# Kernel optimization log

Hardware: AMD Instinct MI355X
Metric: run time of the kernel (lower is better)

Reference implementation:

```python
import jax, jax.numpy as jnp
import numpy as np

NHID = 128
NLAYERS = 4
DT = 1.0
ALPHA = 1.0
GAMMA = 1.0


def setup_inputs() -> dict:
    key = jax.random.key(0)
    k1, k2, k3, k4, k5, k6 = jax.random.split(key, 6)
    N, E = 100000, 1600000
    stdv = 1.0 / np.sqrt(NHID)
    x = jax.random.normal(k1, (N, NHID), dtype=jnp.float32)
    edge_index = jax.random.randint(k2, (2, E), 0, N, dtype=jnp.int64)
    # GCNConv.lin weight (no bias) and separate conv bias; reset_params uniform(-stdv, stdv) for weights
    W = jax.random.uniform(k3, (NHID, NHID), jnp.float32, -stdv, stdv)
    b = jnp.zeros((NHID,), jnp.float32)
    Wres = jax.random.uniform(k4, (NHID, NHID), jnp.float32, -stdv, stdv)
    bres = jax.random.uniform(k5, (NHID,), jnp.float32, -stdv, stdv)
    return {"x": x, "edge_index": edge_index, "W": W, "b": b, "Wres": Wres, "bres": bres}


def reference(x, edge_index, W, b, Wres, bres):
    N = x.shape[0]
    src, dst = edge_index[0], edge_index[1]
    # GCN degree normalization with self-loops (A_hat = A + I)
    deg = jax.ops.segment_sum(jnp.ones(src.shape[0], x.dtype), dst, num_segments=N) + 1.0
    dinv = jax.lax.rsqrt(deg)  # deg >= 1 from self-loops

    def conv(X):
        h = X @ W  # lin (no bias)
        norm = (dinv[src] * dinv[dst])[:, None]
        msg = h[src] * norm                      # [E, nhid] gather
        agg = jax.ops.segment_sum(msg, dst, num_segments=N)  # scatter-add
        agg = agg + h * (dinv * dinv)[:, None]   # self-loop contribution
        return agg + b

    def residual(X):
        # res_connection_v1: -res(conv.lin(X))
        return -((X @ W) @ Wres + bres)

    # dropout is identity in eval mode
    Y = jnp.tanh(x)
    X = Y
    for _ in range(NLAYERS):
        Y = Y + DT * (jnp.tanh(conv(X) + residual(X)) - ALPHA * Y - GAMMA * X)
        X = X + DT * Y
    return X
```

## Files before the change

### kernel.cpp

```cpp
#include <hip/hip_runtime.h>
#include <hip/hip_bf16.h>
#include <stdint.h>

#define THREADS 256
#define WB 256
#define MAXNB 512
#define NBLK_A 512

typedef unsigned short u16;
typedef unsigned int u32;
using frag_ab = __attribute__((ext_vector_type(8))) short;
using f32x4  = __attribute__((ext_vector_type(4))) float;

static __host__ __device__ inline int imin(int a, int b) { return a < b ? a : b; }

static __device__ inline u16 f2b(float f) {
    u32 u = __builtin_bit_cast(u32, f);
    return (u16)((u + 0x7FFFu + ((u >> 16) & 1u)) >> 16);
}
static __device__ inline float b2f_lo(u32 v) { return __builtin_bit_cast(float, v << 16); }
static __device__ inline float b2f_hi(u32 v) { return __builtin_bit_cast(float, v & 0xFFFF0000u); }

static __device__ inline float tanh_fast(float x) {
    const float e = __builtin_amdgcn_exp2f(x * 2.8853900817779268f);
    return 1.0f - 2.0f * __builtin_amdgcn_rcpf(e + 1.0f);
}

static __device__ inline void fma8(float* a, float w, uint4 v) {
    a[0] = fmaf(w, b2f_lo(v.x), a[0]); a[1] = fmaf(w, b2f_hi(v.x), a[1]);
    a[2] = fmaf(w, b2f_lo(v.y), a[2]); a[3] = fmaf(w, b2f_hi(v.y), a[3]);
    a[4] = fmaf(w, b2f_lo(v.z), a[4]); a[5] = fmaf(w, b2f_hi(v.z), a[5]);
    a[6] = fmaf(w, b2f_lo(v.w), a[6]); a[7] = fmaf(w, b2f_hi(v.w), a[7]);
}

__global__ void k_detect(const int* __restrict__ raw, int* __restrict__ flag) {
    __shared__ int found;
    if (threadIdx.x == 0) found = 0;
    __syncthreads();
    if (raw[2 * threadIdx.x + 1] != 0) atomicOr(&found, 1);
    __syncthreads();
    if (threadIdx.x == 0) *flag = found ? 0 : 1;
}

__global__ __launch_bounds__(256)
void k_bucket_count(const int* __restrict__ raw, int E, int EPB, int NB,
                    const int* __restrict__ flag, int* __restrict__ counts) {
    __shared__ int cnt[MAXNB];
    const int t = threadIdx.x, blk = blockIdx.x;
    for (int i = t; i < NB; i += THREADS) cnt[i] = 0;
    __syncthreads();
    const bool is64 = (*flag != 0);
    const int e0 = blk * EPB, e1 = imin(E, e0 + EPB);
    for (int e = e0 + t; e < e1; e += THREADS) {
        const int d = is64 ? raw[2 * E + 2 * e] : raw[E + e];
        atomicAdd(&cnt[d >> 8], 1);
    }
    __syncthreads();
    for (int i = t; i < NB; i += THREADS) counts[i * NBLK_A + blk] = cnt[i];
}

__global__ void k_chunk_sums(const int* __restrict__ a, int* __restrict__ chunkSum, int L) {
    __shared__ int sm[THREADS];
    const int base = blockIdx.x * 2048 + threadIdx.x * 8;
    int s = 0;
#pragma unroll
    for (int i = 0; i < 8; ++i) { int idx = base + i; if (idx < L) s += a[idx]; }
    sm[threadIdx.x] = s;
    __syncthreads();
    for (int off = THREADS / 2; off > 0; off >>= 1) {
        if (threadIdx.x < off) sm[threadIdx.x] += sm[threadIdx.x + off];
        __syncthreads();
    }
    if (threadIdx.x == 0) chunkSum[blockIdx.x] = sm[0];
}

__global__ void k_scan_offsets(const int* __restrict__ chunkSum, int* __restrict__ chunkOff,
                               int nChunks) {
    if (blockIdx.x == 0 && threadIdx.x == 0) {
        int run = 0;
        for (int i = 0; i < nChunks; ++i) { chunkOff[i] = run; run += chunkSum[i]; }
    }
}

__global__ void k_scan_write(int* __restrict__ a, const int* __restrict__ chunkOff, int L) {
    __shared__ int sm[THREADS];
    const int tid = threadIdx.x;
    const int base = blockIdx.x * 2048 + tid * 8;
    int v[8]; int s = 0;
#pragma unroll
    for (int i = 0; i < 8; ++i) { int idx = base + i; v[i] = (idx < L) ? a[idx] : 0; s += v[i]; }
    const int mysum = s;
    sm[tid] = s;
    __syncthreads();
    for (int off = 1; off < THREADS; off <<= 1) {
        int t = (tid >= off) ? sm[tid - off] : 0;
        __syncthreads();
        sm[tid] += t;
        __syncthreads();
    }
    int run = chunkOff[blockIdx.x] + sm[tid] - mysum;
#pragma unroll
    for (int i = 0; i < 8; ++i) {
        int idx = base + i;
        if (idx < L) { a[idx] = run; run += v[i]; }
    }
}

__global__ __launch_bounds__(256)
void k_bucket_scatter(const int* __restrict__ raw, int E, int EPB, int NB,
                      const int* __restrict__ flag, const int* __restrict__ offs,
                      uint2* __restrict__ pairs) {
    __shared__ int cur[MAXNB];
    const int t = threadIdx.x, blk = blockIdx.x;
    for (int i = t; i < NB; i += THREADS) cur[i] = offs[i * NBLK_A + blk];
    __syncthreads();
    const bool is64 = (*flag != 0);
    const int e0 = blk * EPB, e1 = imin(E, e0 + EPB);
    for (int e = e0 + t; e < e1; e += THREADS) {
        int s, d;
        if (is64) { s = raw[2 * e]; d = raw[2 * E + 2 * e]; }
        else      { s = raw[e];     d = raw[E + e]; }
        const int p = atomicAdd(&cur[d >> 8], 1);
        pairs[p] = make_uint2((u32)s, (u32)d);
    }
}

__global__ __launch_bounds__(256)
void k_build(const uint2* __restrict__ pairs, const int* __restrict__ offs,
             int* __restrict__ rowptr, int* __restrict__ csr_src,
             float* __restrict__ dinv, int N, int NB, int E) {
    __shared__ int deg[WB];
    __shared__ int ptr[WB];
    __shared__ int cur[WB];
    const int k = blockIdx.x, t = threadIdx.x;
    const int base = offs[k * NBLK_A];
    const int end  = (k + 1 < NB) ? offs[(k + 1) * NBLK_A] : E;
    const int n0 = k * WB;
    deg[t] = 0;
    __syncthreads();
    for (int e = base + t; e < end; e += THREADS)
        atomicAdd(&deg[(int)pairs[e].y - n0], 1);
    __syncthreads();
    const int dv = deg[t];
    if (n0 + t < N) dinv[n0 + t] = rsqrtf((float)dv + 1.0f);
    ptr[t] = dv;
    __syncthreads();
    for (int off = 1; off < THREADS; off <<= 1) {
        int v = (t >= off) ? ptr[t - off] : 0;
        __syncthreads();
        ptr[t] += v;
        __syncthreads();
    }
    const int excl = ptr[t] - dv;
    if (n0 + t < N) rowptr[n0 + t] = base + excl;
    if (k == NB - 1 && t == 0) rowptr[N] = E;
    cur[t] = excl;
    __syncthreads();
    for (int e = base + t; e < end; e += THREADS) {
        const uint2 pr = pairs[e];
        const int p = atomicAdd(&cur[(int)pr.y - n0], 1);
        csr_src[base + p] = (int)pr.x;
    }
}

__global__ void k_w2(const float* __restrict__ W, const float* __restrict__ Wres,
                     const float* __restrict__ b, const float* __restrict__ bres,
                     u16* __restrict__ Bt, float* __restrict__ cvec) {
    const int gid = blockIdx.x * blockDim.x + threadIdx.x;
    if (gid < 128 * 128) {
        const int i = gid >> 7, n = gid & 127;
        float s = 0.f;
#pragma unroll 8
        for (int k = 0; k < 128; ++k) s += W[i * 128 + k] * Wres[k * 128 + n];
        Bt[n * 256 + 128 + i] = f2b(-s);
        Bt[n * 256 + i]       = f2b(W[i * 128 + n]);
    }
    if (gid < 128) cvec[gid] = b[gid] - bres[gid];
}

__global__ void k_tanh0(const float* __restrict__ x, u16* __restrict__ Xh, long long n4) {
    long long i = blockIdx.x * (long long)blockDim.x + threadIdx.x;
    const long long stride = gridDim.x * (long long)blockDim.x;
    for (; i < n4; i += stride) {
        float4 v = ((const float4*)x)[i];
        u32 lo = f2b(tanh_fast(v.x)) | ((u32)f2b(tanh_fast(v.y)) << 16);
        u32 hi = f2b(tanh_fast(v.z)) | ((u32)f2b(tanh_fast(v.w)) << 16);
        ((uint2*)Xh)[i] = make_uint2(lo, hi);
    }
}

__global__ __launch_bounds__(256)
void k_agg(const u16* __restrict__ Xh, const int* __restrict__ rowptr,
           const int* __restrict__ csr_src, const float* __restrict__ dinv,
           u16* __restrict__ Ph, int N) {
    const int wid = threadIdx.x >> 6;
    const int lane = threadIdx.x & 63;
    const int node = blockIdx.x * 4 + wid;
    if (node >= N) return;
    const int q = lane >> 4;
    const int c8 = (lane & 15) * 8;
    const float dn = dinv[node];
    float acc[8] = {0.f, 0.f, 0.f, 0.f, 0.f, 0.f, 0.f, 0.f};
    const int e0 = rowptr[node], e1 = rowptr[node + 1];
    if (q == 0) {
        const uint4 v = *(const uint4*)&Xh[(size_t)node * 128 + c8];
        fma8(acc, dn, v);
    }
    int e = e0 + q;
    for (; e + 12 < e1; e += 16) {
        const int s0 = csr_src[e];
        const int s1 = csr_src[e + 4];
        const int s2 = csr_src[e + 8];
        const int s3 = csr_src[e + 12];
        const float w0 = dinv[s0], w1 = dinv[s1], w2 = dinv[s2], w3 = dinv[s3];
        const uint4 v0 = *(const uint4*)&Xh[(size_t)s0 * 128 + c8];
        const uint4 v1 = *(const uint4*)&Xh[(size_t)s1 * 128 + c8];
        const uint4 v2 = *(const uint4*)&Xh[(size_t)s2 * 128 + c8];
        const uint4 v3 = *(const uint4*)&Xh[(size_t)s3 * 128 + c8];
        fma8(acc, w0, v0);
        fma8(acc, w1, v1);
        fma8(acc, w2, v2);
        fma8(acc, w3, v3);
    }
    for (; e < e1; e += 4) {
        const int s0 = csr_src[e];
        const float w0 = dinv[s0];
        const uint4 v0 = *(const uint4*)&Xh[(size_t)s0 * 128 + c8];
        fma8(acc, w0, v0);
    }
#pragma unroll
    for (int j = 0; j < 8; ++j) acc[j] += __shfl_xor(acc[j], 16);
#pragma unroll
    for (int j = 0; j < 8; ++j) acc[j] += __shfl_xor(acc[j], 32);
    if (q == 0) {
        u32 w0 = (u32)f2b(acc[0] * dn) | ((u32)f2b(acc[1] * dn) << 16);
        u32 w1 = (u32)f2b(acc[2] * dn) | ((u32)f2b(acc[3] * dn) << 16);
        u32 w2 = (u32)f2b(acc[4] * dn) | ((u32)f2b(acc[5] * dn) << 16);
        u32 w3 = (u32)f2b(acc[6] * dn) | ((u32)f2b(acc[7] * dn) << 16);
        *(uint4*)&Ph[(size_t)node * 128 + c8] = make_uint4(w0, w1, w2, w3);
    }
}

static __device__ inline int swz(int row, int byteInRow) {
    return byteInRow ^ ((row & 7) << 4);
}

__global__ __launch_bounds__(256)
void k_gemm_mfma(const u16* __restrict__ Ph, const u16* __restrict__ Xh,
                 const u16* __restrict__ Bt, const float* __restrict__ cvec,
                 float* __restrict__ Xout, u16* __restrict__ XhOut, int M, int writeF32) {
    __shared__ u16 Bs[128 * 256];
    const int tid = threadIdx.x;

#pragma unroll
    for (int p = 0; p < 16; ++p) {
        const int c = p * 256 + tid;
        const int row = c >> 5, col16 = c & 31;
        const uint4 v = *(const uint4*)&Bt[row * 256 + col16 * 8];
        *(uint4*)&Bs[row * 256 + (swz(row, col16 * 16) >> 1)] = v;
    }

    const int wid = tid >> 6;
    const int lane = tid & 63;
    const int rowbase = blockIdx.x * 128 + wid * 32;
    const int rl = lane & 15;
    const int kg = (lane >> 4) * 8;

    const int r0 = rowbase + rl;
    const size_t ar0 = (size_t)((r0      < M) ? r0      : M - 1);
    const size_t ar1 = (size_t)((r0 + 16 < M) ? r0 + 16 : M - 1);

    frag_ab a0[8], a1[8];
#pragma unroll
    for (int ks = 0; ks < 4; ++ks) {
        const int kk = ks * 32 + kg;
        a0[ks]     = *(const frag_ab*)&Ph[ar0 * 128 + kk];
        a1[ks]     = *(const frag_ab*)&Ph[ar1 * 128 + kk];
        a0[ks + 4] = *(const frag_ab*)&Xh[ar0 * 128 + kk];
        a1[ks + 4] = *(const frag_ab*)&Xh[ar1 * 128 + kk];
    }

    f32x4 acc[2][8];
#pragma unroll
    for (int i = 0; i < 2; ++i)
#pragma unroll
        for (int j = 0; j < 8; ++j) acc[i][j] = (f32x4){0.f, 0.f, 0.f, 0.f};

    __syncthreads();

#pragma unroll
    for (int ks = 0; ks < 8; ++ks) {
        const int kbyte = ks * 64 + (kg * 2);
#pragma unroll
        for (int nf = 0; nf < 8; ++nf) {
            const int r = nf * 16 + rl;
            const frag_ab bv = *(const frag_ab*)&Bs[r * 256 + (swz(r, kbyte) >> 1)];
            acc[0][nf] = __builtin_amdgcn_mfma_f32_16x16x32_bf16(a0[ks], bv, acc[0][nf], 0, 0, 0);
            acc[1][nf] = __builtin_amdgcn_mfma_f32_16x16x32_bf16(a1[ks], bv, acc[1][nf], 0, 0, 0);
        }
    }

    const int rq = (lane >> 4) * 4;
#pragma unroll
    for (int mf = 0; mf < 2; ++mf) {
#pragma unroll
        for (int nf = 0; nf < 8; ++nf) {
            const int c = nf * 16 + rl;
            const float cv = cvec[c];
#pragma unroll
            for (int reg = 0; reg < 4; ++reg) {
                const int r = rowbase + mf * 16 + rq + reg;
                if (r < M) {
                    const float v = tanh_fast(acc[mf][nf][reg] + cv);
                    if (writeF32) Xout[(size_t)r * 128 + c] = v;
                    else          XhOut[(size_t)r * 128 + c] = f2b(v);
                }
            }
        }
    }
}

extern "C" void kernel_launch(void* const* d_in, const int* in_sizes, int n_in,
                              void* d_out, int out_size, void* d_ws, size_t ws_size,
                              hipStream_t stream) {
    const float* x    = (const float*)d_in[0];
    const int*   ei   = (const int*)d_in[1];
    const float* W    = (const float*)d_in[2];
    const float* b    = (const float*)d_in[3];
    const float* Wres = (const float*)d_in[4];
    const float* bres = (const float*)d_in[5];
    const int N = in_sizes[0] / 128;
    const int E = in_sizes[1] / 2;
    float* X = (float*)d_out;

    uint8_t* base = (uint8_t*)d_ws;
    size_t off = 0;
    auto carve = [&](size_t bytes) -> void* {
        void* p = base + off;
        off += (bytes + 255) & ~(size_t)255;
        return p;
    };
    const int NB = imin((N + WB - 1) / WB, MAXNB);
    const int L = NB * NBLK_A;

    u16*   Xh       = (u16*)carve((size_t)N * 128 * sizeof(u16));
    u16*   Ph       = (u16*)carve((size_t)N * 128 * sizeof(u16));
    uint2* pairs    = (uint2*)carve((size_t)E * sizeof(uint2));
    int*   csr_src  = (int*)carve((size_t)E * sizeof(int));
    int*   counts   = (int*)carve((size_t)L * sizeof(int));
    int*   rowptr   = (int*)carve(((size_t)N + 1) * sizeof(int));
    float* dinv     = (float*)carve((size_t)N * sizeof(float));
    u16*   Bt       = (u16*)carve(128 * 256 * sizeof(u16));
    float* cvec     = (float*)carve(128 * sizeof(float));
    int*   chunkSum = (int*)carve(4096);
    int*   chunkOff = (int*)carve(4096);
    int*   flag     = (int*)carve(256);

    const int EPB = (E + NBLK_A - 1) / NBLK_A;
    const int nChunks = (L + 2047) / 2048;

    k_detect<<<1, 256, 0, stream>>>(ei, flag);
    k_bucket_count<<<NBLK_A, THREADS, 0, stream>>>(ei, E, EPB, NB, flag, counts);
    k_chunk_sums<<<nChunks, THREADS, 0, stream>>>(counts, chunkSum, L);
    k_scan_offsets<<<1, 64, 0, stream>>>(chunkSum, chunkOff, nChunks);
    k_scan_write<<<nChunks, THREADS, 0, stream>>>(counts, chunkOff, L);
    k_bucket_scatter<<<NBLK_A, THREADS, 0, stream>>>(ei, E, EPB, NB, flag, counts, pairs);
    k_build<<<NB, THREADS, 0, stream>>>(pairs, counts, rowptr, csr_src, dinv, N, NB, E);
    k_w2<<<64, THREADS, 0, stream>>>(W, Wres, b, bres, Bt, cvec);

    const long long n4 = (long long)N * 32;
    const int tgrid = imin((int)((n4 + THREADS - 1) / THREADS), 2048);
    k_tanh0<<<tgrid, THREADS, 0, stream>>>(x, Xh, n4);

    for (int l = 0; l < 4; ++l) {
        k_agg<<<(N + 3) / 4, THREADS, 0, stream>>>(Xh, rowptr, csr_src, dinv, Ph, N);
        k_gemm_mfma<<<(N + 127) / 128, THREADS, 0, stream>>>(Ph, Xh, Bt, cvec, X, Xh, N,
                                                             (l == 3) ? 1 : 0);
    }
}
```

Measured before the change: 456.4 us.

## Pack edge weights into CSR, one node per 16 lanes, halve GEMM LDS, stage stores

```diff
diff --git a/kernel.cpp b/kernel.cpp
--- a/kernel.cpp
+++ b/kernel.cpp
@@ -33,23 +33,23 @@
     a[6] = fmaf(w, b2f_lo(v.w), a[6]); a[7] = fmaf(w, b2f_hi(v.w), a[7]);
 }
 
-__global__ void k_detect(const int* __restrict__ raw, int* __restrict__ flag) {
-    __shared__ int found;
-    if (threadIdx.x == 0) found = 0;
-    __syncthreads();
-    if (raw[2 * threadIdx.x + 1] != 0) atomicOr(&found, 1);
-    __syncthreads();
-    if (threadIdx.x == 0) *flag = found ? 0 : 1;
+static __device__ inline bool detect64(const int* raw) {
+    __shared__ int s64;
+    if (threadIdx.x == 0) s64 = 1;
+    __syncthreads();
+    if (raw[2 * threadIdx.x + 1] != 0) s64 = 0;
+    __syncthreads();
+    return s64 != 0;
 }
 
 __global__ __launch_bounds__(256)
 void k_bucket_count(const int* __restrict__ raw, int E, int EPB, int NB,
-                    const int* __restrict__ flag, int* __restrict__ counts) {
+                    int* __restrict__ counts) {
+    const bool is64 = detect64(raw);
     __shared__ int cnt[MAXNB];
     const int t = threadIdx.x, blk = blockIdx.x;
     for (int i = t; i < NB; i += THREADS) cnt[i] = 0;
     __syncthreads();
-    const bool is64 = (*flag != 0);
     const int e0 = blk * EPB, e1 = imin(E, e0 + EPB);
     for (int e = e0 + t; e < e1; e += THREADS) {
         const int d = is64 ? raw[2 * E + 2 * e] : raw[E + e];
@@ -108,13 +108,12 @@
 
 __global__ __launch_bounds__(256)
 void k_bucket_scatter(const int* __restrict__ raw, int E, int EPB, int NB,
-                      const int* __restrict__ flag, const int* __restrict__ offs,
-                      uint2* __restrict__ pairs) {
+                      const int* __restrict__ offs, uint2* __restrict__ pairs) {
+    const bool is64 = detect64(raw);
     __shared__ int cur[MAXNB];
     const int t = threadIdx.x, blk = blockIdx.x;
     for (int i = t; i < NB; i += THREADS) cur[i] = offs[i * NBLK_A + blk];
     __syncthreads();
-    const bool is64 = (*flag != 0);
     const int e0 = blk * EPB, e1 = imin(E, e0 + EPB);
     for (int e = e0 + t; e < e1; e += THREADS) {
         int s, d;
@@ -163,6 +162,16 @@
     }
 }
 
+__global__ void k_wfill(const int* __restrict__ csr_src, const float* __restrict__ dinv,
+                        uint2* __restrict__ csrW, int E) {
+    int i = blockIdx.x * blockDim.x + threadIdx.x;
+    const int st = gridDim.x * blockDim.x;
+    for (; i < E; i += st) {
+        const int s = csr_src[i];
+        csrW[i] = make_uint2((u32)s, __builtin_bit_cast(u32, dinv[s]));
+    }
+}
+
 __global__ void k_w2(const float* __restrict__ W, const float* __restrict__ Wres,
                      const float* __restrict__ b, const float* __restrict__ bres,
                      u16* __restrict__ Bt, float* __restrict__ cvec) {
@@ -191,48 +200,39 @@
 
 __global__ __launch_bounds__(256)
 void k_agg(const u16* __restrict__ Xh, const int* __restrict__ rowptr,
-           const int* __restrict__ csr_src, const float* __restrict__ dinv,
-           u16* __restrict__ Ph, int N) {
-    const int wid = threadIdx.x >> 6;
-    const int lane = threadIdx.x & 63;
-    const int node = blockIdx.x * 4 + wid;
-    if (node >= N) return;
-    const int q = lane >> 4;
-    const int c8 = (lane & 15) * 8;
-    const float dn = dinv[node];
+           const uint2* __restrict__ csrW, u16* __restrict__ Ph, int N) {
+    const int qid = threadIdx.x >> 4;
+    const int l16 = threadIdx.x & 15;
+    const int node = blockIdx.x * 16 + qid;
+    const bool valid = node < N;
+    const int c8 = l16 * 8;
+    int e0 = 0, e1 = 0;
+    if (valid) { e0 = rowptr[node]; e1 = rowptr[node + 1]; }
+    const float dn = rsqrtf((float)(e1 - e0) + 1.0f);
     float acc[8] = {0.f, 0.f, 0.f, 0.f, 0.f, 0.f, 0.f, 0.f};
-    const int e0 = rowptr[node], e1 = rowptr[node + 1];
-    if (q == 0) {
+    if (valid) {
         const uint4 v = *(const uint4*)&Xh[(size_t)node * 128 + c8];
         fma8(acc, dn, v);
     }
-    int e = e0 + q;
-    for (; e + 12 < e1; e += 16) {
-        const int s0 = csr_src[e];
-        const int s1 = csr_src[e + 4];
-        const int s2 = csr_src[e + 8];
-        const int s3 = csr_src[e + 12];
-        const float w0 = dinv[s0], w1 = dinv[s1], w2 = dinv[s2], w3 = dinv[s3];
-        const uint4 v0 = *(const uint4*)&Xh[(size_t)s0 * 128 + c8];
-        const uint4 v1 = *(const uint4*)&Xh[(size_t)s1 * 128 + c8];
-        const uint4 v2 = *(const uint4*)&Xh[(size_t)s2 * 128 + c8];
-        const uint4 v3 = *(const uint4*)&Xh[(size_t)s3 * 128 + c8];
-        fma8(acc, w0, v0);
-        fma8(acc, w1, v1);
-        fma8(acc, w2, v2);
-        fma8(acc, w3, v3);
-    }
-    for (; e < e1; e += 4) {
-        const int s0 = csr_src[e];
-        const float w0 = dinv[s0];
-        const uint4 v0 = *(const uint4*)&Xh[(size_t)s0 * 128 + c8];
-        fma8(acc, w0, v0);
-    }
-#pragma unroll
-    for (int j = 0; j < 8; ++j) acc[j] += __shfl_xor(acc[j], 16);
-#pragma unroll
-    for (int j = 0; j < 8; ++j) acc[j] += __shfl_xor(acc[j], 32);
-    if (q == 0) {
+    int e = e0;
+    for (; e + 3 < e1; e += 4) {
+        const uint2 cw0 = csrW[e],     cw1 = csrW[e + 1];
+        const uint2 cw2 = csrW[e + 2], cw3 = csrW[e + 3];
+        const uint4 v0 = *(const uint4*)&Xh[(size_t)cw0.x * 128 + c8];
+        const uint4 v1 = *(const uint4*)&Xh[(size_t)cw1.x * 128 + c8];
+        const uint4 v2 = *(const uint4*)&Xh[(size_t)cw2.x * 128 + c8];
+        const uint4 v3 = *(const uint4*)&Xh[(size_t)cw3.x * 128 + c8];
+        fma8(acc, __builtin_bit_cast(float, cw0.y), v0);
+        fma8(acc, __builtin_bit_cast(float, cw1.y), v1);
+        fma8(acc, __builtin_bit_cast(float, cw2.y), v2);
+        fma8(acc, __builtin_bit_cast(float, cw3.y), v3);
+    }
+    for (; e < e1; ++e) {
+        const uint2 cw = csrW[e];
+        const uint4 v = *(const uint4*)&Xh[(size_t)cw.x * 128 + c8];
+        fma8(acc, __builtin_bit_cast(float, cw.y), v);
+    }
+    if (valid) {
         u32 w0 = (u32)f2b(acc[0] * dn) | ((u32)f2b(acc[1] * dn) << 16);
         u32 w1 = (u32)f2b(acc[2] * dn) | ((u32)f2b(acc[3] * dn) << 16);
         u32 w2 = (u32)f2b(acc[4] * dn) | ((u32)f2b(acc[5] * dn) << 16);
@@ -241,27 +241,13 @@
     }
 }
 
-static __device__ inline int swz(int row, int byteInRow) {
-    return byteInRow ^ ((row & 7) << 4);
-}
-
 __global__ __launch_bounds__(256)
 void k_gemm_mfma(const u16* __restrict__ Ph, const u16* __restrict__ Xh,
                  const u16* __restrict__ Bt, const float* __restrict__ cvec,
                  float* __restrict__ Xout, u16* __restrict__ XhOut, int M, int writeF32) {
-    __shared__ u16 Bs[128 * 256];
+    __shared__ u16 Bs[128 * 128];
     const int tid = threadIdx.x;
-
-#pragma unroll
-    for (int p = 0; p < 16; ++p) {
-        const int c = p * 256 + tid;
-        const int row = c >> 5, col16 = c & 31;
-        const uint4 v = *(const uint4*)&Bt[row * 256 + col16 * 8];
-        *(uint4*)&Bs[row * 256 + (swz(row, col16 * 16) >> 1)] = v;
-    }
-
-    const int wid = tid >> 6;
-    const int lane = tid & 63;
+    const int wid = tid >> 6, lane = tid & 63;
     const int rowbase = blockIdx.x * 128 + wid * 32;
     const int rl = lane & 15;
     const int kg = (lane >> 4) * 8;
@@ -286,35 +272,69 @@
 #pragma unroll
         for (int j = 0; j < 8; ++j) acc[i][j] = (f32x4){0.f, 0.f, 0.f, 0.f};
 
-    __syncthreads();
-
-#pragma unroll
-    for (int ks = 0; ks < 8; ++ks) {
-        const int kbyte = ks * 64 + (kg * 2);
-#pragma unroll
-        for (int nf = 0; nf < 8; ++nf) {
-            const int r = nf * 16 + rl;
-            const frag_ab bv = *(const frag_ab*)&Bs[r * 256 + (swz(r, kbyte) >> 1)];
-            acc[0][nf] = __builtin_amdgcn_mfma_f32_16x16x32_bf16(a0[ks], bv, acc[0][nf], 0, 0, 0);
-            acc[1][nf] = __builtin_amdgcn_mfma_f32_16x16x32_bf16(a1[ks], bv, acc[1][nf], 0, 0, 0);
+#pragma unroll 1
+    for (int half = 0; half < 2; ++half) {
+#pragma unroll
+        for (int p = 0; p < 8; ++p) {
+            const int c = p * 256 + tid;
+            const int row = c >> 4, c16 = c & 15;
+            const uint4 v = *(const uint4*)&Bt[row * 256 + half * 128 + c16 * 8];
+            *(uint4*)&Bs[row * 128 + (((c16 * 16) ^ ((row & 7) << 4)) >> 1)] = v;
         }
+        __syncthreads();
+#pragma unroll
+        for (int ks = 0; ks < 4; ++ks) {
+            const int kb = ks * 64 + kg * 2;
+#pragma unroll
+            for (int nf = 0; nf < 8; ++nf) {
+                const int r = nf * 16 + rl;
+                const frag_ab bv = *(const frag_ab*)&Bs[r * 128 + ((kb ^ ((r & 7) << 4)) >> 1)];
+                acc[0][nf] = __builtin_amdgcn_mfma_f32_16x16x32_bf16(a0[half * 4 + ks], bv,
+                                                                      acc[0][nf], 0, 0, 0);
+                acc[1][nf] = __builtin_amdgcn_mfma_f32_16x16x32_bf16(a1[half * 4 + ks], bv,
+                                                                      acc[1][nf], 0, 0, 0);
+            }
+        }
+        __syncthreads();
     }
 
     const int rq = (lane >> 4) * 4;
-#pragma unroll
-    for (int mf = 0; mf < 2; ++mf) {
-#pragma unroll
-        for (int nf = 0; nf < 8; ++nf) {
-            const int c = nf * 16 + rl;
-            const float cv = cvec[c];
-#pragma unroll
-            for (int reg = 0; reg < 4; ++reg) {
-                const int r = rowbase + mf * 16 + rq + reg;
-                if (r < M) {
-                    const float v = tanh_fast(acc[mf][nf][reg] + cv);
-                    if (writeF32) Xout[(size_t)r * 128 + c] = v;
-                    else          XhOut[(size_t)r * 128 + c] = f2b(v);
+    if (writeF32) {
+#pragma unroll
+        for (int mf = 0; mf < 2; ++mf)
+#pragma unroll
+            for (int nf = 0; nf < 8; ++nf) {
+                const int c = nf * 16 + rl;
+                const float cv = cvec[c];
+#pragma unroll
+                for (int reg = 0; reg < 4; ++reg) {
+                    const int r = rowbase + mf * 16 + rq + reg;
+                    if (r < M) Xout[(size_t)r * 128 + c] = tanh_fast(acc[mf][nf][reg] + cv);
                 }
+            }
+    } else {
+#pragma unroll
+        for (int mf = 0; mf < 2; ++mf)
+#pragma unroll
+            for (int nf = 0; nf < 8; ++nf) {
+                const int c = nf * 16 + rl;
+                const float cv = cvec[c];
+#pragma unroll
+                for (int reg = 0; reg < 4; ++reg) {
+                    const int rloc = wid * 32 + mf * 16 + rq + reg;
+                    Bs[rloc * 128 + (c ^ ((rloc & 7) << 3))] =
+                        f2b(tanh_fast(acc[mf][nf][reg] + cv));
+                }
+            }
+        __syncthreads();
+#pragma unroll
+        for (int k = 0; k < 8; ++k) {
+            const int ci = k * 256 + tid;
+            const int row = ci >> 4, c8 = ci & 15;
+            const int gr = blockIdx.x * 128 + row;
+            if (gr < M) {
+                const uint4 v = *(const uint4*)&Bs[row * 128 + ((c8 * 8) ^ ((row & 7) << 3))];
+                *(uint4*)&XhOut[(size_t)gr * 128 + c8 * 8] = v;
             }
         }
     }
@@ -346,6 +366,7 @@
     u16*   Xh       = (u16*)carve((size_t)N * 128 * sizeof(u16));
     u16*   Ph       = (u16*)carve((size_t)N * 128 * sizeof(u16));
     uint2* pairs    = (uint2*)carve((size_t)E * sizeof(uint2));
+    uint2* csrW     = pairs;
     int*   csr_src  = (int*)carve((size_t)E * sizeof(int));
     int*   counts   = (int*)carve((size_t)L * sizeof(int));
     int*   rowptr   = (int*)carve(((size_t)N + 1) * sizeof(int));
@@ -354,18 +375,17 @@
     float* cvec     = (float*)carve(128 * sizeof(float));
     int*   chunkSum = (int*)carve(4096);
     int*   chunkOff = (int*)carve(4096);
-    int*   flag     = (int*)carve(256);
 
     const int EPB = (E + NBLK_A - 1) / NBLK_A;
     const int nChunks = (L + 2047) / 2048;
 
-    k_detect<<<1, 256, 0, stream>>>(ei, flag);
-    k_bucket_count<<<NBLK_A, THREADS, 0, stream>>>(ei, E, EPB, NB, flag, counts);
+    k_bucket_count<<<NBLK_A, THREADS, 0, stream>>>(ei, E, EPB, NB, counts);
     k_chunk_sums<<<nChunks, THREADS, 0, stream>>>(counts, chunkSum, L);
     k_scan_offsets<<<1, 64, 0, stream>>>(chunkSum, chunkOff, nChunks);
     k_scan_write<<<nChunks, THREADS, 0, stream>>>(counts, chunkOff, L);
-    k_bucket_scatter<<<NBLK_A, THREADS, 0, stream>>>(ei, E, EPB, NB, flag, counts, pairs);
+    k_bucket_scatter<<<NBLK_A, THREADS, 0, stream>>>(ei, E, EPB, NB, counts, pairs);
     k_build<<<NB, THREADS, 0, stream>>>(pairs, counts, rowptr, csr_src, dinv, N, NB, E);
+    k_wfill<<<2048, THREADS, 0, stream>>>(csr_src, dinv, csrW, E);
     k_w2<<<64, THREADS, 0, stream>>>(W, Wres, b, bres, Bt, cvec);
 
     const long long n4 = (long long)N * 32;
@@ -373,7 +393,7 @@
     k_tanh0<<<tgrid, THREADS, 0, stream>>>(x, Xh, n4);
 
     for (int l = 0; l < 4; ++l) {
-        k_agg<<<(N + 3) / 4, THREADS, 0, stream>>>(Xh, rowptr, csr_src, dinv, Ph, N);
+        k_agg<<<(N + 15) / 16, THREADS, 0, stream>>>(Xh, rowptr, csrW, Ph, N);
         k_gemm_mfma<<<(N + 127) / 128, THREADS, 0, stream>>>(Ph, Xh, Bt, cvec, X, Xh, N,
                                                              (l == 3) ? 1 : 0);
     }
```

New measurement: 963.4 us. 2.11x slower.
